# Kernel tuning notes

Measured on AMD Instinct MI355X. Metric: run time of the kernel, lower is better.

The kernel has to match this reference:

```python
import jax, jax.numpy as jnp
import numpy as np
import math

B, C, HH, WW = 4, 256, 64, 64
NUM_HEADS = 4
GROUPS = 8
EPS = 1e-5


def setup_inputs() -> dict:
    key = jax.random.key(0)
    k1, k2, k3 = jax.random.split(key, 3)
    x = jax.random.normal(k1, (B, C, HH, WW), dtype=jnp.float32)
    gn_w = jnp.ones((C,), dtype=jnp.float32)
    gn_b = jnp.zeros((C,), dtype=jnp.float32)
    qkv_w = jax.random.normal(k2, (3 * C, C), dtype=jnp.float32) * (1.0 / math.sqrt(C))
    qkv_b = jnp.zeros((3 * C,), dtype=jnp.float32)
    proj_w = jax.random.normal(k3, (C, C), dtype=jnp.float32) * (1.0 / math.sqrt(C))
    proj_b = jnp.zeros((C,), dtype=jnp.float32)
    return {"x": x, "gn_w": gn_w, "gn_b": gn_b, "qkv_w": qkv_w,
            "qkv_b": qkv_b, "proj_w": proj_w, "proj_b": proj_b}


def reference(x, gn_w, gn_b, qkv_w, qkv_b, proj_w, proj_b):
    b, c, h, w = x.shape
    nh = NUM_HEADS
    d = c // nh          # head dim = 64
    s = h * w            # sequence length = 4096

    # GroupNorm(8, c): normalize over (c//G, h, w) per group, biased variance
    xg = x.reshape(b, GROUPS, c // GROUPS, h, w)
    mu = xg.mean(axis=(2, 3, 4), keepdims=True)
    var = xg.var(axis=(2, 3, 4), keepdims=True)
    xn = ((xg - mu) * jax.lax.rsqrt(var + EPS)).reshape(b, c, h, w)
    xn = xn * gn_w[None, :, None, None] + gn_b[None, :, None, None]

    # 1x1 conv QKV == channel-wise matmul
    qkv = jnp.einsum('oc,bchw->bohw', qkv_w, xn) + qkv_b[None, :, None, None]
    qkv = qkv.reshape(b, 3, nh, d, s)
    q = jnp.transpose(qkv[:, 0], (0, 1, 3, 2))  # [b, nh, s, d]
    k = jnp.transpose(qkv[:, 1], (0, 1, 3, 2))
    v = jnp.transpose(qkv[:, 2], (0, 1, 3, 2))

    scale = 1.0 / math.sqrt(d)
    attn = jnp.einsum('bhqd,bhkd->bhqk', q, k) * scale  # [b, nh, s, s]
    attn = jax.nn.softmax(attn, axis=-1)
    out = jnp.einsum('bhqk,bhkd->bhqd', attn, v)        # [b, nh, s, d]

    out = jnp.transpose(out, (0, 1, 3, 2)).reshape(b, c, h, w)
    out = jnp.einsum('oc,bchw->bohw', proj_w, out) + proj_b[None, :, None, None]
    return out + x
```

## Files before the change

### kernel.cpp

```cpp
#include <hip/hip_runtime.h>
#include <hip/hip_bf16.h>

#define B_ 4
#define C_ 256
#define S_ 4096
#define NH_ 4
#define HD_ 64
#define LOG2E 1.4426950408889634f
#define QSC 0.18033688011112042f

typedef __attribute__((ext_vector_type(8))) short short8;
typedef __attribute__((ext_vector_type(4))) short short4v;
typedef __attribute__((ext_vector_type(4))) float f32x4;
typedef __attribute__((ext_vector_type(16))) float f32x16;
typedef __attribute__((ext_vector_type(4))) unsigned uint4v;

static __device__ __forceinline__ short f2bf(float f) {
  unsigned u = __builtin_bit_cast(unsigned, f);
  u += 0x7fffu + ((u >> 16) & 1u);
  return (short)(u >> 16);
}
static __device__ __forceinline__ float bf2f(short h) {
  unsigned u = ((unsigned)(unsigned short)h) << 16;
  return __builtin_bit_cast(float, u);
}

#if __has_builtin(__builtin_amdgcn_exp2f)
#define EXP2(x) __builtin_amdgcn_exp2f(x)
#else
#define EXP2(x) exp2f(x)
#endif

static __device__ __forceinline__ unsigned pkbf(float a, float b) {
  unsigned r;
  asm("v_cvt_pk_bf16_f32 %0, %1, %2" : "=v"(r) : "v"(a), "v"(b));
  return r;
}
static __device__ __forceinline__ void pl32swap(unsigned& a, unsigned& b) {
  asm volatile("v_permlane32_swap_b32 %0, %1" : "+v"(a), "+v"(b));
}
static __device__ __forceinline__ void gl_lds16(const short* g, char* l) {
  __builtin_amdgcn_global_load_lds(
      (const __attribute__((address_space(1))) void*)g,
      (__attribute__((address_space(3))) void*)l, 16, 0, 0);
}

__global__ __launch_bounds__(256) void k_gn_part(const float* __restrict__ x,
                                                 float* __restrict__ part) {
  const float* p = x + (size_t)blockIdx.x * 16384;
  int t = threadIdx.x;
  float s = 0.f, ss = 0.f;
  const float4* p4 = reinterpret_cast<const float4*>(p);
  for (int i = t; i < 4096; i += 256) {
    float4 v = p4[i];
    s += v.x + v.y + v.z + v.w;
    ss += v.x * v.x + v.y * v.y + v.z * v.z + v.w * v.w;
  }
  for (int m = 1; m < 64; m <<= 1) {
    s += __shfl_xor(s, m, 64);
    ss += __shfl_xor(ss, m, 64);
  }
  __shared__ float rs[4], rss[4];
  int w = t >> 6;
  if ((t & 63) == 0) { rs[w] = s; rss[w] = ss; }
  __syncthreads();
  if (t == 0) {
    part[2 * blockIdx.x] = rs[0] + rs[1] + rs[2] + rs[3];
    part[2 * blockIdx.x + 1] = rss[0] + rss[1] + rss[2] + rss[3];
  }
}

__global__ void k_gn_fin(const float* __restrict__ part, float* __restrict__ stats) {
  int t = threadIdx.x;
  if (t < 32) {
    float s = 0.f, ss = 0.f;
    for (int j = 0; j < 8; j++) {
      s += part[2 * (t * 8 + j)];
      ss += part[2 * (t * 8 + j) + 1];
    }
    float inv = 1.f / (32.f * S_);
    float mu = s * inv;
    float var = ss * inv - mu * mu;
    stats[t] = mu;
    stats[32 + t] = rsqrtf(var + 1e-5f);
  }
}

__global__ __launch_bounds__(256) void k_wconv(const float* __restrict__ wq,
                                               const float* __restrict__ wp,
                                               short* __restrict__ oq,
                                               short* __restrict__ op) {
  int i = (blockIdx.x * 256 + threadIdx.x) * 4;
  const int n1 = 768 * 256;
  float sc = 1.f;
  const float* src;
  short* dst;
  if (i < n1) {
    src = wq + i; dst = oq + i;
    if (i < 256 * 256) sc = QSC;
  } else {
    src = wp + (i - n1); dst = op + (i - n1);
  }
  float4 v = *reinterpret_cast<const float4*>(src);
  short4v o;
  o[0] = f2bf(v.x * sc); o[1] = f2bf(v.y * sc);
  o[2] = f2bf(v.z * sc); o[3] = f2bf(v.w * sc);
  *reinterpret_cast<short4v*>(dst) = o;
}

__global__ __launch_bounds__(256) void k_gn_apply(const float* __restrict__ x,
                                                  const float* __restrict__ gw,
                                                  const float* __restrict__ gb,
                                                  const float* __restrict__ stats,
                                                  short* __restrict__ xnt) {
  int st = blockIdx.x;
  int ct = blockIdx.y;
  int b = blockIdx.z;
  int t = threadIdx.x;
  __shared__ short T[64 * 72];
  int c0 = ct * 64, s0 = st * 64;
  int r4 = t >> 4;
  int f4 = t & 15;
  for (int p = 0; p < 4; p++) {
    int r = p * 16 + r4;
    int c = c0 + r;
    float mu = stats[b * 8 + (c >> 5)];
    float ri = stats[32 + b * 8 + (c >> 5)];
    float A = gw[c] * ri;
    float Bb = gb[c] - mu * A;
    float4 v = *reinterpret_cast<const float4*>(x + ((size_t)(b * C_ + c)) * S_ + s0 + f4 * 4);
    int sb = f4 * 4;
    T[(sb + 0) * 72 + r] = f2bf(v.x * A + Bb);
    T[(sb + 1) * 72 + r] = f2bf(v.y * A + Bb);
    T[(sb + 2) * 72 + r] = f2bf(v.z * A + Bb);
    T[(sb + 3) * 72 + r] = f2bf(v.w * A + Bb);
  }
  __syncthreads();
  for (int it = 0; it < 2; it++) {
    int cch = t + it * 256;
    int sl = cch >> 3, c8 = cch & 7;
    short8 v = *reinterpret_cast<short8*>(&T[sl * 72 + c8 * 8]);
    *reinterpret_cast<short8*>(xnt + ((size_t)(b * S_ + s0 + sl)) * C_ + c0 + c8 * 8) = v;
  }
}

template <int MODE>
__global__ __launch_bounds__(256) void k_gemm(const short* __restrict__ Wbf,
                                              const short* __restrict__ Xt,
                                              const float* __restrict__ bias,
                                              const float* __restrict__ xres,
                                              short* __restrict__ q_sd,
                                              short* __restrict__ k_sd,
                                              short* __restrict__ v_ds,
                                              const short* __restrict__ op1g,
                                              const float* __restrict__ lbufg,
                                              float* __restrict__ outp) {
  int tn = blockIdx.x;
  int tm = blockIdx.y;
  int b = blockIdx.z;
  int t = threadIdx.x;
  __shared__ short lds[4 * 64 * 72];
  short* Al = lds;
  short* Bl = lds + 128 * 40;
  int w = t >> 6, lane = t & 63;
  int wr = w >> 1, wc = w & 1;
  int l15 = lane & 15, l4 = lane >> 4;

  f32x4 acc[4][4];
  for (int m = 0; m < 4; m++)
    for (int n = 0; n < 4; n++)
      for (int j = 0; j < 4; j++) acc[m][n][j] = 0.f;

  const short* Arow = Wbf + (size_t)(tm * 128) * 256;
  const short* Brow = Xt + ((size_t)b * S_ + tn * 128) * 256;

  for (int kk = 0; kk < 256; kk += 32) {
    __syncthreads();
    for (int i = 0; i < 2; i++) {
      int cch = t + i * 256;
      int r = cch >> 2, c4 = cch & 3;
      short8 va = *reinterpret_cast<const short8*>(Arow + (size_t)r * 256 + kk + c4 * 8);
      *reinterpret_cast<short8*>(&Al[r * 40 + c4 * 8]) = va;
      short8 vbv;
      if (MODE == 0) {
        vbv = *reinterpret_cast<const short8*>(Brow + (size_t)r * 256 + kk + c4 * 8);
      } else {
        int c = kk + c4 * 8;
        int bh2 = b * 4 + (c >> 6);
        int d = c & 63;
        int s_glob = tn * 128 + r;
        size_t ro = ((size_t)bh2 * S_ + s_glob) * HD_ + d;
        short8 p0 = *reinterpret_cast<const short8*>(Xt + ro);
        short8 p1 = *reinterpret_cast<const short8*>(op1g + ro);
        float l0 = lbufg[(size_t)bh2 * S_ + s_glob];
        float l1 = lbufg[(size_t)(16 + bh2) * S_ + s_glob];
        float inv = 1.f / (l0 + l1);
#pragma unroll
        for (int j = 0; j < 8; j++) vbv[j] = f2bf((bf2f(p0[j]) + bf2f(p1[j])) * inv);
      }
      *reinterpret_cast<short8*>(&Bl[r * 40 + c4 * 8]) = vbv;
    }
    __syncthreads();
    short8 af[4], bf[4];
    for (int mt = 0; mt < 4; mt++)
      af[mt] = *reinterpret_cast<short8*>(&Al[(wr * 64 + mt * 16 + l15) * 40 + l4 * 8]);
    for (int nt = 0; nt < 4; nt++)
      bf[nt] = *reinterpret_cast<short8*>(&Bl[(wc * 64 + nt * 16 + l15) * 40 + l4 * 8]);
    for (int mt = 0; mt < 4; mt++)
      for (int nt = 0; nt < 4; nt++)
        acc[mt][nt] = __builtin_amdgcn_mfma_f32_16x16x32_bf16(af[mt], bf[nt], acc[mt][nt], 0, 0, 0);
  }
  __syncthreads();

  if (MODE == 0) {
    int o_base = tm * 128 + wr * 64;
    int tt = o_base >> 8;
    int h = (o_base >> 6) & 3;
    int s_base = tn * 128 + wc * 64;
    int bh = b * NH_ + h;
    if (tt == 2) {
      for (int mt = 0; mt < 4; mt++)
        for (int nt = 0; nt < 4; nt++)
          for (int i = 0; i < 4; i++) {
            int o = o_base + mt * 16 + l4 * 4 + i;
            int dd = o & 63;
            int s = s_base + nt * 16 + l15;
            float val = acc[mt][nt][i] + bias[o];
            v_ds[((size_t)bh * HD_ + dd) * S_ + s] = f2bf(val);
          }
    } else {
      float bsc = (tt == 0) ? QSC : 1.f;
      short* T = lds + w * (64 * 72);
      for (int mt = 0; mt < 4; mt++)
        for (int nt = 0; nt < 4; nt++)
          for (int i = 0; i < 4; i++) {
            int o = o_base + mt * 16 + l4 * 4 + i;
            int dd = mt * 16 + l4 * 4 + i;
            int sl = nt * 16 + l15;
            float val = acc[mt][nt][i] + bias[o] * bsc;
            T[sl * 72 + dd] = f2bf(val);
          }
      short* dst = (tt == 0) ? q_sd : k_sd;
      for (int it = 0; it < 8; it++) {
        int cch = lane + it * 64;
        int sl = cch >> 3, c8 = cch & 7;
        short8 v = *reinterpret_cast<short8*>(&T[sl * 72 + c8 * 8]);
        *reinterpret_cast<short8*>(dst + ((size_t)bh * S_ + s_base + sl) * HD_ + c8 * 8) = v;
      }
    }
  } else {
    for (int mt = 0; mt < 4; mt++) {
      int o = tm * 128 + wr * 64 + mt * 16 + l4 * 4;
      for (int nt = 0; nt < 4; nt++) {
        int s = tn * 128 + wc * 64 + nt * 16 + l15;
        for (int i = 0; i < 4; i++) {
          size_t off = ((size_t)(b * C_ + o + i)) * S_ + s;
          outp[off] = acc[mt][nt][i] + bias[o + i] + xres[off];
        }
      }
    }
  }
}

__global__ __launch_bounds__(256, 2) void k_attn(const short* __restrict__ q_sd,
                                                 const short* __restrict__ k_sd,
                                                 const short* __restrict__ v_ds,
                                                 short* __restrict__ op_base,
                                                 long op_stride,
                                                 float* __restrict__ lbuf,
                                                 int ntile) {
  int bid = blockIdx.x;
  int qt = bid >> 5;
  int bh = (bid >> 1) & 15;
  int sk = bid & 1;
  int t = threadIdx.x, w = t >> 6, lane = t & 63;
  int l31 = lane & 31, hi = lane >> 5, hi8 = hi * 8;
  int qb = qt * 256 + w * 64;

  __shared__ char smem[32768];

  int wb = __builtin_amdgcn_readfirstlane(w) << 10;

  int r8 = t >> 3, s8 = t & 7;
  int sw8 = (s8 ^ (r8 & 7)) * 8;
  const short* kb = k_sd + ((size_t)bh * S_ + (size_t)sk * ntile * 64) * HD_;
  const short* vbg = v_ds + (size_t)bh * HD_ * S_ + sk * ntile * 64;
  int koff0 = r8 * 64 + sw8;
  int koff1 = koff0 + 32 * 64;
  size_t voff0 = (size_t)r8 * S_ + sw8;
  size_t voff1 = voff0 + (size_t)32 * S_;

#define STAGE(bsel, ti)                                                        \
  do {                                                                         \
    const short* kt_ = kb + (size_t)(ti) * (64 * HD_);                         \
    const short* vt_ = vbg + (ti) * 64;                                        \
    char* lb_ = smem + ((bsel) << 14) + wb;                                    \
    gl_lds16(kt_ + koff0, lb_);                                                \
    gl_lds16(kt_ + koff1, lb_ + 4096);                                         \
    gl_lds16(vt_ + voff0, lb_ + 8192);                                         \
    gl_lds16(vt_ + voff1, lb_ + 12288);                                        \
  } while (0)

  const short* qpA = q_sd + ((size_t)bh * S_ + qb + l31) * HD_ + hi8;
  short8 qfA[4], qfB[4];
#pragma unroll
  for (int sl = 0; sl < 4; sl++) {
    qfA[sl] = *reinterpret_cast<const short8*>(qpA + sl * 16);
    qfB[sl] = *reinterpret_cast<const short8*>(qpA + 32 * HD_ + sl * 16);
  }

  int x7 = l31 & 7;
  int rb0 = l31 * 128;

  f32x16 OA0, OA1, OB0, OB1;
#pragma unroll
  for (int r = 0; r < 16; r++) { OA0[r] = 0.f; OA1[r] = 0.f; OB0[r] = 0.f; OB1[r] = 0.f; }
  float lA = 0.f, lB = 0.f;

  STAGE(0, 0);
  if (ntile > 1) STAGE(1, 1);
  asm volatile("s_waitcnt vmcnt(0)" ::: "memory");
  __builtin_amdgcn_s_barrier();
  asm volatile("" ::: "memory");

#define MKPA(pa, s0, s1)                                                       \
  do {                                                                         \
    unsigned c0 = pkbf(s0[0], s0[1]), c1 = pkbf(s0[2], s0[3]);                 \
    unsigned c2 = pkbf(s0[4], s0[5]), c3 = pkbf(s0[6], s0[7]);                 \
    pl32swap(c0, c2); pl32swap(c1, c3);                                        \
    uint4v u0; u0[0] = c0; u0[1] = c1; u0[2] = c2; u0[3] = c3;                 \
    pa[0] = __builtin_bit_cast(short8, u0);                                    \
    unsigned c4 = pkbf(s0[8], s0[9]), c5 = pkbf(s0[10], s0[11]);               \
    unsigned c6 = pkbf(s0[12], s0[13]), c7 = pkbf(s0[14], s0[15]);             \
    pl32swap(c4, c6); pl32swap(c5, c7);                                        \
    uint4v u1; u1[0] = c4; u1[1] = c5; u1[2] = c6; u1[3] = c7;                 \
    pa[1] = __builtin_bit_cast(short8, u1);                                    \
    unsigned d0 = pkbf(s1[0], s1[1]), d1 = pkbf(s1[2], s1[3]);                 \
    unsigned d2 = pkbf(s1[4], s1[5]), d3 = pkbf(s1[6], s1[7]);                 \
    pl32swap(d0, d2); pl32swap(d1, d3);                                        \
    uint4v u2; u2[0] = d0; u2[1] = d1; u2[2] = d2; u2[3] = d3;                 \
    pa[2] = __builtin_bit_cast(short8, u2);                                    \
    unsigned d4 = pkbf(s1[8], s1[9]), d5 = pkbf(s1[10], s1[11]);               \
    unsigned d6 = pkbf(s1[12], s1[13]), d7 = pkbf(s1[14], s1[15]);             \
    pl32swap(d4, d6); pl32swap(d5, d7);                                        \
    uint4v u3; u3[0] = d4; u3[1] = d5; u3[2] = d6; u3[3] = d7;                 \
    pa[3] = __builtin_bit_cast(short8, u3);                                    \
  } while (0)

  for (int it = 0; it < ntile; it++) {
    char* cur = smem + ((it & 1) << 14);

    f32x16 sA0, sA1, sB0, sB1;
#pragma unroll
    for (int r = 0; r < 16; r++) { sA0[r] = 0.f; sA1[r] = 0.f; sB0[r] = 0.f; sB1[r] = 0.f; }
    __builtin_amdgcn_s_setprio(1);
#pragma unroll
    for (int sl = 0; sl < 4; sl++) {
      int so = ((sl * 2 + hi) ^ x7) << 4;
      short8 kf0 = *reinterpret_cast<short8*>(cur + rb0 + so);
      short8 kf1 = *reinterpret_cast<short8*>(cur + 4096 + rb0 + so);
      sA0 = __builtin_amdgcn_mfma_f32_32x32x16_bf16(kf0, qfA[sl], sA0, 0, 0, 0);
      sB0 = __builtin_amdgcn_mfma_f32_32x32x16_bf16(kf0, qfB[sl], sB0, 0, 0, 0);
      sA1 = __builtin_amdgcn_mfma_f32_32x32x16_bf16(kf1, qfA[sl], sA1, 0, 0, 0);
      sB1 = __builtin_amdgcn_mfma_f32_32x32x16_bf16(kf1, qfB[sl], sB1, 0, 0, 0);
    }
    __builtin_amdgcn_s_setprio(0);

#pragma unroll
    for (int r = 0; r < 16; r++) sA0[r] = EXP2(sA0[r]);
#pragma unroll
    for (int r = 0; r < 16; r++) sA1[r] = EXP2(sA1[r]);
#pragma unroll
    for (int r = 0; r < 16; r++) sB0[r] = EXP2(sB0[r]);
#pragma unroll
    for (int r = 0; r < 16; r++) sB1[r] = EXP2(sB1[r]);
    {
      float a0 = 0.f, a1 = 0.f, a2 = 0.f, a3 = 0.f;
      float b0 = 0.f, b1 = 0.f, b2 = 0.f, b3 = 0.f;
#pragma unroll
      for (int r = 0; r < 16; r += 4) {
        a0 += sA0[r]; a1 += sA0[r + 1]; a2 += sA0[r + 2]; a3 += sA0[r + 3];
        a0 += sA1[r]; a1 += sA1[r + 1]; a2 += sA1[r + 2]; a3 += sA1[r + 3];
        b0 += sB0[r]; b1 += sB0[r + 1]; b2 += sB0[r + 2]; b3 += sB0[r + 3];
        b0 += sB1[r]; b1 += sB1[r + 1]; b2 += sB1[r + 2]; b3 += sB1[r + 3];
      }
      float rsA = (a0 + a1) + (a2 + a3);
      float rsB = (b0 + b1) + (b2 + b3);
      rsA += __shfl_xor(rsA, 32, 64);
      rsB += __shfl_xor(rsB, 32, 64);
      lA += rsA;
      lB += rsB;
    }

    short8 paA[4], paB[4];
    MKPA(paA, sA0, sA1);
    MKPA(paB, sB0, sB1);

    __builtin_amdgcn_s_setprio(1);
#pragma unroll
    for (int ks = 0; ks < 4; ks++) {
      int so = ((ks * 2 + hi) ^ x7) << 4;
      short8 vf0 = *reinterpret_cast<short8*>(cur + 8192 + rb0 + so);
      short8 vf1 = *reinterpret_cast<short8*>(cur + 12288 + rb0 + so);
      OA0 = __builtin_amdgcn_mfma_f32_32x32x16_bf16(vf0, paA[ks], OA0, 0, 0, 0);
      OB0 = __builtin_amdgcn_mfma_f32_32x32x16_bf16(vf0, paB[ks], OB0, 0, 0, 0);
      OA1 = __builtin_amdgcn_mfma_f32_32x32x16_bf16(vf1, paA[ks], OA1, 0, 0, 0);
      OB1 = __builtin_amdgcn_mfma_f32_32x32x16_bf16(vf1, paB[ks], OB1, 0, 0, 0);
    }
    __builtin_amdgcn_s_setprio(0);

    if (it + 1 < ntile) {
      __builtin_amdgcn_s_barrier();
      if (it + 2 < ntile) {
        STAGE(it & 1, it + 2);
        asm volatile("s_waitcnt vmcnt(4)" ::: "memory");
      } else {
        asm volatile("s_waitcnt vmcnt(0)" ::: "memory");
      }
      __builtin_amdgcn_s_barrier();
      asm volatile("" ::: "memory");
    }
  }

  short* optrA = op_base + (size_t)sk * op_stride + ((size_t)bh * S_ + qb + l31) * HD_;
  short* optrB = optrA + 32 * HD_;
#pragma unroll
  for (int qd = 0; qd < 4; qd++) {
    short4v a0, a1, b0v, b1v;
#pragma unroll
    for (int i = 0; i < 4; i++) {
      a0[i] = f2bf(OA0[qd * 4 + i]);
      a1[i] = f2bf(OA1[qd * 4 + i]);
      b0v[i] = f2bf(OB0[qd * 4 + i]);
      b1v[i] = f2bf(OB1[qd * 4 + i]);
    }
    int d0 = qd * 8 + hi * 4;
    *reinterpret_cast<short4v*>(optrA + d0) = a0;
    *reinterpret_cast<short4v*>(optrA + 32 + d0) = a1;
    *reinterpret_cast<short4v*>(optrB + d0) = b0v;
    *reinterpret_cast<short4v*>(optrB + 32 + d0) = b1v;
  }
  if (hi == 0) {
    lbuf[(size_t)(sk * 16 + bh) * S_ + qb + l31] = lA;
    lbuf[(size_t)(sk * 16 + bh) * S_ + qb + 32 + l31] = lB;
  }
#undef STAGE
#undef MKPA
}

extern "C" void kernel_launch(void* const* d_in, const int* in_sizes, int n_in,
                              void* d_out, int out_size, void* d_ws, size_t ws_size,
                              hipStream_t stream) {
  const float* x      = (const float*)d_in[0];
  const float* gn_w   = (const float*)d_in[1];
  const float* gn_b   = (const float*)d_in[2];
  const float* qkv_w  = (const float*)d_in[3];
  const float* qkv_b  = (const float*)d_in[4];
  const float* proj_w = (const float*)d_in[5];
  const float* proj_b = (const float*)d_in[6];
  char* ws = (char*)d_ws;
  float* stats = (float*)(ws + 0);
  float* part  = (float*)(ws + 2048);
  short* wqkv  = (short*)(ws + 4096);
  short* wproj = (short*)(ws + 397312);
  short* xnt   = (short*)(ws + 528384);
  short* q_sd  = (short*)(ws + 8916992);
  short* k_sd  = (short*)(ws + 17305600);
  short* v_ds  = (short*)(ws + 25694208);
  short* op0   = xnt;
  short* op1   = (short*)(ws + 42471424);
  long op_stride = (42471424 - 528384) / 2;
  float* lbuf  = (float*)(ws + 50860032);
  float* outp  = (float*)d_out;

  k_gn_part<<<256, 256, 0, stream>>>(x, part);
  k_gn_fin<<<1, 64, 0, stream>>>(part, stats);
  k_wconv<<<256, 256, 0, stream>>>(qkv_w, proj_w, wqkv, wproj);
  k_gn_apply<<<dim3(64, 4, 4), 256, 0, stream>>>(x, gn_w, gn_b, stats, xnt);
  k_gemm<0><<<dim3(32, 6, 4), 256, 0, stream>>>(wqkv, xnt, qkv_b, nullptr, q_sd, k_sd, v_ds,
                                                nullptr, nullptr, nullptr);
  k_attn<<<512, 256, 0, stream>>>(q_sd, k_sd, v_ds, op0, op_stride, lbuf, 32);
  k_gemm<1><<<dim3(32, 2, 4), 256, 0, stream>>>(wproj, op0, proj_b, x, nullptr, nullptr, nullptr,
                                                op1, lbuf, outp);
}
```

Before: 130.2 us.

## Split attention KV into four chunks and fuse GroupNorm prep kernels

When the workspace is large enough, attention splits the key/value sequence four ways instead of two, launching 1024 blocks instead of 512. The projection GEMM then sums the four partial outputs and their softmax denominators. Separately, the weight bf16 conversion is merged into the GroupNorm partial-sum kernel, and the stats finalisation moves into the apply kernel, which removes two launches. In exchange, the split writes more partial-output traffic and the projection does more reduction work.

```diff
diff --git a/kernel.cpp b/kernel.cpp
--- a/kernel.cpp
+++ b/kernel.cpp
@@ -45,10 +45,14 @@
       (__attribute__((address_space(3))) void*)l, 16, 0, 0);
 }
 
-__global__ __launch_bounds__(256) void k_gn_part(const float* __restrict__ x,
-                                                 float* __restrict__ part) {
+__global__ __launch_bounds__(256) void k_pre(const float* __restrict__ x,
+                                             const float* __restrict__ wq,
+                                             const float* __restrict__ wp,
+                                             float* __restrict__ part,
+                                             short* __restrict__ oq,
+                                             short* __restrict__ op) {
+  int t = threadIdx.x;
   const float* p = x + (size_t)blockIdx.x * 16384;
-  int t = threadIdx.x;
   float s = 0.f, ss = 0.f;
   const float4* p4 = reinterpret_cast<const float4*>(p);
   for (int i = t; i < 4096; i += 256) {
@@ -63,6 +67,24 @@
   __shared__ float rs[4], rss[4];
   int w = t >> 6;
   if ((t & 63) == 0) { rs[w] = s; rss[w] = ss; }
+  {
+    int i = (blockIdx.x * 256 + t) * 4;
+    const int n1 = 768 * 256;
+    float sc = 1.f;
+    const float* src;
+    short* dst;
+    if (i < n1) {
+      src = wq + i; dst = oq + i;
+      if (i < 256 * 256) sc = QSC;
+    } else {
+      src = wp + (i - n1); dst = op + (i - n1);
+    }
+    float4 v = *reinterpret_cast<const float4*>(src);
+    short4v o;
+    o[0] = f2bf(v.x * sc); o[1] = f2bf(v.y * sc);
+    o[2] = f2bf(v.z * sc); o[3] = f2bf(v.w * sc);
+    *reinterpret_cast<short4v*>(dst) = o;
+  }
   __syncthreads();
   if (t == 0) {
     part[2 * blockIdx.x] = rs[0] + rs[1] + rs[2] + rs[3];
@@ -70,62 +92,41 @@
   }
 }
 
-__global__ void k_gn_fin(const float* __restrict__ part, float* __restrict__ stats) {
-  int t = threadIdx.x;
-  if (t < 32) {
-    float s = 0.f, ss = 0.f;
-    for (int j = 0; j < 8; j++) {
-      s += part[2 * (t * 8 + j)];
-      ss += part[2 * (t * 8 + j) + 1];
-    }
-    float inv = 1.f / (32.f * S_);
-    float mu = s * inv;
-    float var = ss * inv - mu * mu;
-    stats[t] = mu;
-    stats[32 + t] = rsqrtf(var + 1e-5f);
-  }
-}
-
-__global__ __launch_bounds__(256) void k_wconv(const float* __restrict__ wq,
-                                               const float* __restrict__ wp,
-                                               short* __restrict__ oq,
-                                               short* __restrict__ op) {
-  int i = (blockIdx.x * 256 + threadIdx.x) * 4;
-  const int n1 = 768 * 256;
-  float sc = 1.f;
-  const float* src;
-  short* dst;
-  if (i < n1) {
-    src = wq + i; dst = oq + i;
-    if (i < 256 * 256) sc = QSC;
-  } else {
-    src = wp + (i - n1); dst = op + (i - n1);
-  }
-  float4 v = *reinterpret_cast<const float4*>(src);
-  short4v o;
-  o[0] = f2bf(v.x * sc); o[1] = f2bf(v.y * sc);
-  o[2] = f2bf(v.z * sc); o[3] = f2bf(v.w * sc);
-  *reinterpret_cast<short4v*>(dst) = o;
-}
-
 __global__ __launch_bounds__(256) void k_gn_apply(const float* __restrict__ x,
                                                   const float* __restrict__ gw,
                                                   const float* __restrict__ gb,
-                                                  const float* __restrict__ stats,
+                                                  const float* __restrict__ part,
                                                   short* __restrict__ xnt) {
   int st = blockIdx.x;
   int ct = blockIdx.y;
   int b = blockIdx.z;
   int t = threadIdx.x;
   __shared__ short T[64 * 72];
+  __shared__ float smu[2], sri[2];
   int c0 = ct * 64, s0 = st * 64;
+  if (t < 2) {
+    int g = (c0 >> 5) + t;
+    int base = b * 64 + g * 8;
+    float s = 0.f, ss = 0.f;
+    for (int j = 0; j < 8; j++) {
+      s += part[2 * (base + j)];
+      ss += part[2 * (base + j) + 1];
+    }
+    float inv = 1.f / (32.f * S_);
+    float mu = s * inv;
+    float var = ss * inv - mu * mu;
+    smu[t] = mu;
+    sri[t] = rsqrtf(var + 1e-5f);
+  }
+  __syncthreads();
   int r4 = t >> 4;
   int f4 = t & 15;
   for (int p = 0; p < 4; p++) {
     int r = p * 16 + r4;
     int c = c0 + r;
-    float mu = stats[b * 8 + (c >> 5)];
-    float ri = stats[32 + b * 8 + (c >> 5)];
+    int gl = r >> 5;
+    float mu = smu[gl];
+    float ri = sri[gl];
     float A = gw[c] * ri;
     float Bb = gb[c] - mu * A;
     float4 v = *reinterpret_cast<const float4*>(x + ((size_t)(b * C_ + c)) * S_ + s0 + f4 * 4);
@@ -144,7 +145,7 @@
   }
 }
 
-template <int MODE>
+template <int MODE, int NSP>
 __global__ __launch_bounds__(256) void k_gemm(const short* __restrict__ Wbf,
                                               const short* __restrict__ Xt,
                                               const float* __restrict__ bias,
@@ -152,7 +153,7 @@
                                               short* __restrict__ q_sd,
                                               short* __restrict__ k_sd,
                                               short* __restrict__ v_ds,
-                                              const short* __restrict__ op1g,
+                                              long op_stride,
                                               const float* __restrict__ lbufg,
                                               float* __restrict__ outp) {
   int tn = blockIdx.x;
@@ -190,13 +191,18 @@
         int d = c & 63;
         int s_glob = tn * 128 + r;
         size_t ro = ((size_t)bh2 * S_ + s_glob) * HD_ + d;
-        short8 p0 = *reinterpret_cast<const short8*>(Xt + ro);
-        short8 p1 = *reinterpret_cast<const short8*>(op1g + ro);
-        float l0 = lbufg[(size_t)bh2 * S_ + s_glob];
-        float l1 = lbufg[(size_t)(16 + bh2) * S_ + s_glob];
-        float inv = 1.f / (l0 + l1);
-#pragma unroll
-        for (int j = 0; j < 8; j++) vbv[j] = f2bf((bf2f(p0[j]) + bf2f(p1[j])) * inv);
+        float a8[8] = {0.f, 0.f, 0.f, 0.f, 0.f, 0.f, 0.f, 0.f};
+        float l = 0.f;
+#pragma unroll
+        for (int i2 = 0; i2 < NSP; i2++) {
+          short8 pv = *reinterpret_cast<const short8*>(Xt + (size_t)i2 * op_stride + ro);
+#pragma unroll
+          for (int j = 0; j < 8; j++) a8[j] += bf2f(pv[j]);
+          l += lbufg[(size_t)(i2 * 16 + bh2) * S_ + s_glob];
+        }
+        float inv = 1.f / l;
+#pragma unroll
+        for (int j = 0; j < 8; j++) vbv[j] = f2bf(a8[j] * inv);
       }
       *reinterpret_cast<short8*>(&Bl[r * 40 + c4 * 8]) = vbv;
     }
@@ -268,11 +274,11 @@
                                                  short* __restrict__ op_base,
                                                  long op_stride,
                                                  float* __restrict__ lbuf,
-                                                 int ntile) {
+                                                 int ntile, int lg) {
   int bid = blockIdx.x;
-  int qt = bid >> 5;
-  int bh = (bid >> 1) & 15;
-  int sk = bid & 1;
+  int sk = bid & ((1 << lg) - 1);
+  int bh = (bid >> lg) & 15;
+  int qt = bid >> (lg + 4);
   int t = threadIdx.x, w = t >> 6, lane = t & 63;
   int l31 = lane & 31, hi = lane >> 5, hi8 = hi * 8;
   int qb = qt * 256 + w * 64;
@@ -459,7 +465,6 @@
   const float* proj_w = (const float*)d_in[5];
   const float* proj_b = (const float*)d_in[6];
   char* ws = (char*)d_ws;
-  float* stats = (float*)(ws + 0);
   float* part  = (float*)(ws + 2048);
   short* wqkv  = (short*)(ws + 4096);
   short* wproj = (short*)(ws + 397312);
@@ -467,19 +472,36 @@
   short* q_sd  = (short*)(ws + 8916992);
   short* k_sd  = (short*)(ws + 17305600);
   short* v_ds  = (short*)(ws + 25694208);
-  short* op0   = xnt;
-  short* op1   = (short*)(ws + 42471424);
-  long op_stride = (42471424 - 528384) / 2;
-  float* lbuf  = (float*)(ws + 50860032);
   float* outp  = (float*)d_out;
 
-  k_gn_part<<<256, 256, 0, stream>>>(x, part);
-  k_gn_fin<<<1, 64, 0, stream>>>(part, stats);
-  k_wconv<<<256, 256, 0, stream>>>(qkv_w, proj_w, wqkv, wproj);
-  k_gn_apply<<<dim3(64, 4, 4), 256, 0, stream>>>(x, gn_w, gn_b, stats, xnt);
-  k_gemm<0><<<dim3(32, 6, 4), 256, 0, stream>>>(wqkv, xnt, qkv_b, nullptr, q_sd, k_sd, v_ds,
-                                                nullptr, nullptr, nullptr);
-  k_attn<<<512, 256, 0, stream>>>(q_sd, k_sd, v_ds, op0, op_stride, lbuf, 32);
-  k_gemm<1><<<dim3(32, 2, 4), 256, 0, stream>>>(wproj, op0, proj_b, x, nullptr, nullptr, nullptr,
-                                                op1, lbuf, outp);
-}
+  const size_t need4 = 42471424ULL + 4ULL * 8388608ULL + 4ULL * 16 * 4096 * 4;
+  int lg;
+  short* op_base;
+  long op_stride;
+  float* lbuf;
+  if (ws_size >= need4) {
+    lg = 2;
+    op_base = (short*)(ws + 42471424);
+    op_stride = 8388608 / 2;
+    lbuf = (float*)(ws + 42471424 + 4ULL * 8388608ULL);
+  } else {
+    lg = 1;
+    op_base = xnt;
+    op_stride = (42471424 - 528384) / 2;
+    lbuf = (float*)(ws + 50860032);
+  }
+  int NS = 1 << lg;
+
+  k_pre<<<256, 256, 0, stream>>>(x, qkv_w, proj_w, part, wqkv, wproj);
+  k_gn_apply<<<dim3(64, 4, 4), 256, 0, stream>>>(x, gn_w, gn_b, part, xnt);
+  k_gemm<0, 0><<<dim3(32, 6, 4), 256, 0, stream>>>(wqkv, xnt, qkv_b, nullptr, q_sd, k_sd, v_ds,
+                                                   0, nullptr, nullptr);
+  k_attn<<<16 * 16 * NS, 256, 0, stream>>>(q_sd, k_sd, v_ds, op_base, op_stride, lbuf,
+                                           64 >> lg, lg);
+  if (NS == 4)
+    k_gemm<1, 4><<<dim3(32, 2, 4), 256, 0, stream>>>(wproj, op_base, proj_b, x, nullptr, nullptr,
+                                                     nullptr, op_stride, lbuf, outp);
+  else
+    k_gemm<1, 2><<<dim3(32, 2, 4), 256, 0, stream>>>(wproj, op_base, proj_b, x, nullptr, nullptr,
+                                                     nullptr, op_stride, lbuf, outp);
+}
```

New measurement: 135.1 us. 3.7% more time.
